# Optimization experiments

Measured on AMD Instinct MI355X. Metric: run time of the kernel, lower is better.

## Reference

```python
import jax, jax.numpy as jnp
import numpy as np
import math

INPUT_SIZE = 512
DK = 64
B, N = 8, 2048

def setup_inputs() -> dict:
    key = jax.random.key(0)
    k1, k2, k3, k4, k5, k6 = jax.random.split(key, 6)
    X = jax.random.normal(k1, (B, N, INPUT_SIZE), dtype=jnp.float32)
    h = jax.random.normal(k2, (B, N, INPUT_SIZE), dtype=jnp.float32)
    s = 1.0 / math.sqrt(INPUT_SIZE)
    WQ = jax.random.uniform(k3, (INPUT_SIZE, DK), dtype=jnp.float32, minval=-s, maxval=s)
    bQ = jax.random.uniform(k4, (DK,), dtype=jnp.float32, minval=-s, maxval=s)
    WK = jax.random.uniform(k5, (INPUT_SIZE, DK), dtype=jnp.float32, minval=-s, maxval=s)
    bK = jax.random.uniform(k6, (DK,), dtype=jnp.float32, minval=-s, maxval=s)
    return {"X": X, "h": h, "WQ": WQ, "bQ": bQ, "WK": WK, "bK": bK}

def reference(X, h, WQ, bQ, WK, bK):
    # Q = linearQ(h), K = linearK(X); dropout is eval-mode identity
    Q = jnp.einsum('bnd,dk->bnk', h, WQ) + bQ   # [B, N, dk]
    K = jnp.einsum('bnd,dk->bnk', X, WK) + bK   # [B, N, dk]
    scores = jnp.einsum('bqk,bnk->bqn', Q, K) / jnp.sqrt(jnp.asarray(DK, X.dtype))
    A = jax.nn.softmax(scores, axis=-1)          # [B, N, N]
    out = jnp.einsum('bqn,bnd->bqd', A, X)       # V = X
    return out
```

## Files before the change

kernel.cpp:

```cpp
#include <hip/hip_runtime.h>
#include <hip/hip_bf16.h>

#define B_ 8
#define N_ 2048
#define D_ 512
#define DK_ 64

typedef float f32x4 __attribute__((ext_vector_type(4)));
typedef short bf16x8 __attribute__((ext_vector_type(8)));
typedef unsigned short u16;

__device__ __forceinline__ u16 f2bf(float f) {
  union { float f; unsigned u; } v; v.f = f;
  unsigned r = v.u + 0x7FFFu + ((v.u >> 16) & 1u);
  return (u16)(r >> 16);
}

#define MFMA16(a, b, cacc) __builtin_amdgcn_mfma_f32_16x16x32_bf16((a), (b), (cacc), 0, 0, 0)


__global__ __launch_bounds__(256) void vt_kernel(const float* __restrict__ X,
                                                 u16* __restrict__ Vf) {
  int bid = blockIdx.x;
  int dt = bid & 7, nt = (bid >> 3) & 31, b = bid >> 8;
  int n0 = nt * 64, d0 = dt * 64;
  __shared__ u16 T[64 * 72];
  int t = threadIdx.x;
  const float* Xb = X + ((size_t)b * N_ + n0) * D_ + d0;
#pragma unroll
  for (int p = 0; p < 4; ++p) {
    int r = p * 16 + (t >> 4);
    int c4 = (t & 15) * 4;
    f32x4 v = *reinterpret_cast<const f32x4*>(Xb + (size_t)r * D_ + c4);
#pragma unroll
    for (int j = 0; j < 4; ++j) T[(c4 + j) * 72 + r] = f2bf(v[j]);
  }
  __syncthreads();
  int w = t >> 6, l = t & 63, g = l >> 4, c = l & 15;
#pragma unroll
  for (int ks = 0; ks < 2; ++ks) {
    bf16x8 v = *reinterpret_cast<const bf16x8*>(&T[(w * 16 + c) * 72 + ks * 32 + 8 * g]);
    *reinterpret_cast<bf16x8*>(
        Vf + (((size_t)(b * 32 + dt * 4 + w) * 32 + nt) * 2 + ks) * 512 + l * 8) = v;
  }
}

__global__ __launch_bounds__(256) void proj_kernel(
    const float* __restrict__ h, const float* __restrict__ X,
    const float* __restrict__ WQ, const float* __restrict__ bQ,
    const float* __restrict__ WK, const float* __restrict__ bK,
    u16* __restrict__ Qf, u16* __restrict__ Kf) {
  int bid = blockIdx.x;
  int b = bid & 7, nt = bid >> 3;
  int n0 = nt * 64;
  int t = threadIdx.x, w = t >> 6, l = t & 63, g = l >> 4, c = l & 15;
  int arow = n0 + w * 16 + c;
  const float* hrow = h + ((size_t)b * N_ + arow) * D_;
  const float* Xrow = X + ((size_t)b * N_ + arow) * D_;
  f32x4 accq[4], acck[4];
#pragma unroll
  for (int cf = 0; cf < 4; ++cf) {
    accq[cf] = (f32x4){0.f, 0.f, 0.f, 0.f};
    acck[cf] = (f32x4){0.f, 0.f, 0.f, 0.f};
  }
  for (int k0 = 0; k0 < D_; k0 += 32) {
    bf16x8 ah, ax;
    {
      f32x4 h0 = *reinterpret_cast<const f32x4*>(hrow + k0 + 8 * g);
      f32x4 h1 = *reinterpret_cast<const f32x4*>(hrow + k0 + 8 * g + 4);
      f32x4 x0 = *reinterpret_cast<const f32x4*>(Xrow + k0 + 8 * g);
      f32x4 x1 = *reinterpret_cast<const f32x4*>(Xrow + k0 + 8 * g + 4);
#pragma unroll
      for (int i = 0; i < 4; ++i) {
        ah[i] = (short)f2bf(h0[i]); ah[i + 4] = (short)f2bf(h1[i]);
        ax[i] = (short)f2bf(x0[i]); ax[i + 4] = (short)f2bf(x1[i]);
      }
    }
#pragma unroll
    for (int cf = 0; cf < 4; ++cf) {
      bf16x8 bq, bk;
#pragma unroll
      for (int i = 0; i < 8; ++i) {
        int kk = k0 + 8 * g + i;
        bq[i] = (short)f2bf(WQ[(size_t)kk * DK_ + cf * 16 + c]);
        bk[i] = (short)f2bf(WK[(size_t)kk * DK_ + cf * 16 + c]);
      }
      accq[cf] = MFMA16(ah, bq, accq[cf]);
      acck[cf] = MFMA16(ax, bk, acck[cf]);
    }
  }
#pragma unroll
  for (int cf = 0; cf < 4; ++cf) {
    float vq = bQ[cf * 16 + c], vk = bK[cf * 16 + c];
    int ks = cf >> 1;
    int g2 = ((cf & 1) * 16 + c) >> 3;
    int i2 = c & 7;
#pragma unroll
    for (int r = 0; r < 4; ++r) {
      size_t e = ((size_t)(b * 128 + nt * 4 + w) * 2 + ks) * 512 +
                 (g2 * 16 + 4 * g + r) * 8 + i2;
      Qf[e] = f2bf((accq[cf][r] + vq) * 0.125f);
      Kf[e] = f2bf(acck[cf][r] + vk);
    }
  }
}

__global__ __launch_bounds__(512, 1) void attn_kernel(
    const u16* __restrict__ Qf, const u16* __restrict__ Kf,
    const u16* __restrict__ Vf, float* __restrict__ out) {
  int bid = blockIdx.x;
  int b = bid & 7, qt = bid >> 3;
  int q0 = qt * 64;
  int t = threadIdx.x, w = t >> 6, l = t & 63, g = l >> 4, c = l & 15;
  int qh = w >> 2, kq = w & 3;

  __shared__ u16 Plds[2][64][72];
  __shared__ float Lp[4][64];

  bf16x8 aq[2][2];
#pragma unroll
  for (int qf = 0; qf < 2; ++qf)
#pragma unroll
    for (int ks = 0; ks < 2; ++ks)
      aq[qf][ks] = *reinterpret_cast<const bf16x8*>(
          Qf + ((size_t)(b * 128 + qt * 4 + qh * 2 + qf) * 2 + ks) * 512 + l * 8);

  f32x4 o[4][4];
#pragma unroll
  for (int a = 0; a < 4; ++a)
#pragma unroll
    for (int d = 0; d < 4; ++d) o[a][d] = (f32x4){0.f, 0.f, 0.f, 0.f};
  float lp[2][4];
#pragma unroll
  for (int a = 0; a < 2; ++a)
#pragma unroll
    for (int r = 0; r < 4; ++r) lp[a][r] = 0.f;

  const u16* Kbase = Kf + (size_t)(b * 128 + kq) * 2 * 512 + l * 8;
  const u16* Vbase = Vf + ((size_t)(b * 32 + w * 4) * 32) * 2 * 512 + l * 8;

  bf16x8 vA[8], vB[8], kA[2], kB[2];
#pragma unroll
  for (int ks = 0; ks < 2; ++ks) {
    kA[ks] = *reinterpret_cast<const bf16x8*>(Kbase + (size_t)ks * 512);
#pragma unroll
    for (int df = 0; df < 4; ++df)
      vA[ks * 4 + df] = *reinterpret_cast<const bf16x8*>(
          Vbase + ((size_t)df * 32 * 2 + ks) * 512);
  }

  auto body = [&](bf16x8 (&vC)[8], bf16x8 (&kC)[2],
                  bf16x8 (&vN)[8], bf16x8 (&kN)[2], int i) {
    const int pb = i & 1;
    const int kvn = (i + 1) & 31;

#pragma unroll
    for (int ks = 0; ks < 2; ++ks) {
      kN[ks] = *reinterpret_cast<const bf16x8*>(
          Kbase + ((size_t)kvn * 4 * 2 + ks) * 512);
#pragma unroll
      for (int df = 0; df < 4; ++df)
        vN[ks * 4 + df] = *reinterpret_cast<const bf16x8*>(
            Vbase + (((size_t)df * 32 + kvn) * 2 + ks) * 512);
    }

    f32x4 s0 = (f32x4){0.f, 0.f, 0.f, 0.f};
    f32x4 s1 = (f32x4){0.f, 0.f, 0.f, 0.f};
    s0 = MFMA16(aq[0][0], kC[0], s0); s0 = MFMA16(aq[0][1], kC[1], s0);
    s1 = MFMA16(aq[1][0], kC[0], s1); s1 = MFMA16(aq[1][1], kC[1], s1);

#pragma unroll
    for (int r = 0; r < 4; ++r) {
      float p0 = __expf(s0[r]); lp[0][r] += p0;
      Plds[pb][qh * 32 + 4 * g + r][kq * 16 + c] = f2bf(p0);
      float p1 = __expf(s1[r]); lp[1][r] += p1;
      Plds[pb][qh * 32 + 16 + 4 * g + r][kq * 16 + c] = f2bf(p1);
    }

    __syncthreads();

#pragma unroll
    for (int ks = 0; ks < 2; ++ks) {
      bf16x8 pa0 = *reinterpret_cast<const bf16x8*>(&Plds[pb][c][ks * 32 + 8 * g]);
      bf16x8 pa1 = *reinterpret_cast<const bf16x8*>(&Plds[pb][16 + c][ks * 32 + 8 * g]);
      bf16x8 pa2 = *reinterpret_cast<const bf16x8*>(&Plds[pb][32 + c][ks * 32 + 8 * g]);
      bf16x8 pa3 = *reinterpret_cast<const bf16x8*>(&Plds[pb][48 + c][ks * 32 + 8 * g]);
#pragma unroll
      for (int df = 0; df < 4; ++df) {
        o[0][df] = MFMA16(pa0, vC[ks * 4 + df], o[0][df]);
        o[1][df] = MFMA16(pa1, vC[ks * 4 + df], o[1][df]);
        o[2][df] = MFMA16(pa2, vC[ks * 4 + df], o[2][df]);
        o[3][df] = MFMA16(pa3, vC[ks * 4 + df], o[3][df]);
      }
    }
  };

#pragma unroll 1
  for (int i = 0; i < 32; i += 2) {
    body(vA, kA, vB, kB, i);
    body(vB, kB, vA, kA, i + 1);
  }

#pragma unroll
  for (int qf = 0; qf < 2; ++qf)
#pragma unroll
    for (int r = 0; r < 4; ++r) {
      float v = lp[qf][r];
      v += __shfl_xor(v, 1); v += __shfl_xor(v, 2);
      v += __shfl_xor(v, 4); v += __shfl_xor(v, 8);
      lp[qf][r] = v;
    }
  if (c == 0) {
#pragma unroll
    for (int qf = 0; qf < 2; ++qf)
#pragma unroll
      for (int r = 0; r < 4; ++r)
        Lp[kq][qh * 32 + qf * 16 + 4 * g + r] = lp[qf][r];
  }
  __syncthreads();

  float* outb = out + ((size_t)b * N_ + q0) * D_;
#pragma unroll
  for (int qf2 = 0; qf2 < 4; ++qf2)
#pragma unroll
    for (int r = 0; r < 4; ++r) {
      int ql = qf2 * 16 + 4 * g + r;
      float L = Lp[0][ql] + Lp[1][ql] + Lp[2][ql] + Lp[3][ql];
      float inv = 1.0f / L;
#pragma unroll
      for (int df = 0; df < 4; ++df)
        outb[(size_t)ql * D_ + w * 64 + df * 16 + c] = o[qf2][df][r] * inv;
    }
}

extern "C" void kernel_launch(void* const* d_in, const int* in_sizes, int n_in,
                              void* d_out, int out_size, void* d_ws, size_t ws_size,
                              hipStream_t stream) {
  const float* X  = (const float*)d_in[0];
  const float* h  = (const float*)d_in[1];
  const float* WQ = (const float*)d_in[2];
  const float* bQ = (const float*)d_in[3];
  const float* WK = (const float*)d_in[4];
  const float* bK = (const float*)d_in[5];
  float* out = (float*)d_out;

  u16* Vf = (u16*)d_ws;
  u16* Qf = Vf + (size_t)B_ * D_ * N_;
  u16* Kf = Qf + (size_t)B_ * N_ * DK_;

  vt_kernel<<<dim3(2048), dim3(256), 0, stream>>>(X, Vf);
  proj_kernel<<<dim3(256), dim3(256), 0, stream>>>(h, X, WQ, bQ, WK, bK, Qf, Kf);
  attn_kernel<<<dim3(256), dim3(512), 0, stream>>>(Qf, Kf, Vf, out);
}
```

Measured before the change: 81.34 us.

## Compute transposed scores in registers to drop LDS round-trip and barriers for P

```diff
diff --git a/kernel.cpp b/kernel.cpp
--- a/kernel.cpp
+++ b/kernel.cpp
@@ -8,6 +8,9 @@
 
 typedef float f32x4 __attribute__((ext_vector_type(4)));
 typedef short bf16x8 __attribute__((ext_vector_type(8)));
+typedef short bf16x4 __attribute__((ext_vector_type(4)));
+typedef unsigned int uint2v __attribute__((ext_vector_type(2)));
+typedef unsigned long long u64x2 __attribute__((ext_vector_type(2)));
 typedef unsigned short u16;
 
 __device__ __forceinline__ u16 f2bf(float f) {
@@ -16,14 +19,21 @@
   return (u16)(r >> 16);
 }
 
-#define MFMA16(a, b, cacc) __builtin_amdgcn_mfma_f32_16x16x32_bf16((a), (b), (cacc), 0, 0, 0)
+#define MFMA32(a, b, cacc) __builtin_amdgcn_mfma_f32_16x16x32_bf16((a), (b), (cacc), 0, 0, 0)
+#define MFMA16(a, b, cacc) __builtin_amdgcn_mfma_f32_16x16x16bf16_1k((a), (b), (cacc), 0, 0, 0)
+
+__device__ __forceinline__ unsigned cvt_pk_bf16(float lo, float hi) {
+  unsigned r;
+  asm("v_cvt_pk_bf16_f32 %0, %1, %2" : "=v"(r) : "v"(lo), "v"(hi));
+  return r;
+}
 
 
 __global__ __launch_bounds__(256) void vt_kernel(const float* __restrict__ X,
                                                  u16* __restrict__ Vf) {
   int bid = blockIdx.x;
-  int dt = bid & 7, nt = (bid >> 3) & 31, b = bid >> 8;
-  int n0 = nt * 64, d0 = dt * 64;
+  int dt8 = bid & 7, nt = (bid >> 3) & 31, b = bid >> 8;
+  int n0 = nt * 64, d0 = dt8 * 64;
   __shared__ u16 T[64 * 72];
   int t = threadIdx.x;
   const float* Xb = X + ((size_t)b * N_ + n0) * D_ + d0;
@@ -38,10 +48,15 @@
   __syncthreads();
   int w = t >> 6, l = t & 63, g = l >> 4, c = l & 15;
 #pragma unroll
-  for (int ks = 0; ks < 2; ++ks) {
-    bf16x8 v = *reinterpret_cast<const bf16x8*>(&T[(w * 16 + c) * 72 + ks * 32 + 8 * g]);
+  for (int jl = 0; jl < 2; ++jl) {
+    u64x2 tmp;
+    tmp[0] = *reinterpret_cast<const unsigned long long*>(
+        &T[(w * 16 + c) * 72 + jl * 32 + 4 * g]);
+    tmp[1] = *reinterpret_cast<const unsigned long long*>(
+        &T[(w * 16 + c) * 72 + jl * 32 + 16 + 4 * g]);
+    bf16x8 v = __builtin_bit_cast(bf16x8, tmp);
     *reinterpret_cast<bf16x8*>(
-        Vf + (((size_t)(b * 32 + dt * 4 + w) * 32 + nt) * 2 + ks) * 512 + l * 8) = v;
+        Vf + (((size_t)(b * 32 + dt8 * 4 + w) * 64) + nt * 2 + jl) * 512 + l * 8) = v;
   }
 }
 
@@ -85,8 +100,8 @@
         bq[i] = (short)f2bf(WQ[(size_t)kk * DK_ + cf * 16 + c]);
         bk[i] = (short)f2bf(WK[(size_t)kk * DK_ + cf * 16 + c]);
       }
-      accq[cf] = MFMA16(ah, bq, accq[cf]);
-      acck[cf] = MFMA16(ax, bk, acck[cf]);
+      accq[cf] = MFMA32(ah, bq, accq[cf]);
+      acck[cf] = MFMA32(ax, bk, acck[cf]);
     }
   }
 #pragma unroll
@@ -105,131 +120,120 @@
   }
 }
 
-__global__ __launch_bounds__(512, 1) void attn_kernel(
+__global__ __launch_bounds__(512, 2) void attn_kernel(
     const u16* __restrict__ Qf, const u16* __restrict__ Kf,
     const u16* __restrict__ Vf, float* __restrict__ out) {
   int bid = blockIdx.x;
   int b = bid & 7, qt = bid >> 3;
   int q0 = qt * 64;
   int t = threadIdx.x, w = t >> 6, l = t & 63, g = l >> 4, c = l & 15;
-  int qh = w >> 2, kq = w & 3;
-
-  __shared__ u16 Plds[2][64][72];
-  __shared__ float Lp[4][64];
-
-  bf16x8 aq[2][2];
-#pragma unroll
-  for (int qf = 0; qf < 2; ++qf)
+
+  __shared__ float Lsh[8][64];
+
+  bf16x8 aq[4][2];
+#pragma unroll
+  for (int sl = 0; sl < 4; ++sl)
 #pragma unroll
     for (int ks = 0; ks < 2; ++ks)
-      aq[qf][ks] = *reinterpret_cast<const bf16x8*>(
-          Qf + ((size_t)(b * 128 + qt * 4 + qh * 2 + qf) * 2 + ks) * 512 + l * 8);
+      aq[sl][ks] = *reinterpret_cast<const bf16x8*>(
+          Qf + ((size_t)(b * 128 + qt * 4 + sl) * 2 + ks) * 512 + l * 8);
 
   f32x4 o[4][4];
 #pragma unroll
-  for (int a = 0; a < 4; ++a)
-#pragma unroll
-    for (int d = 0; d < 4; ++d) o[a][d] = (f32x4){0.f, 0.f, 0.f, 0.f};
-  float lp[2][4];
-#pragma unroll
-  for (int a = 0; a < 2; ++a)
-#pragma unroll
-    for (int r = 0; r < 4; ++r) lp[a][r] = 0.f;
-
-  const u16* Kbase = Kf + (size_t)(b * 128 + kq) * 2 * 512 + l * 8;
-  const u16* Vbase = Vf + ((size_t)(b * 32 + w * 4) * 32) * 2 * 512 + l * 8;
-
-  bf16x8 vA[8], vB[8], kA[2], kB[2];
-#pragma unroll
-  for (int ks = 0; ks < 2; ++ks) {
-    kA[ks] = *reinterpret_cast<const bf16x8*>(Kbase + (size_t)ks * 512);
-#pragma unroll
-    for (int df = 0; df < 4; ++df)
-      vA[ks * 4 + df] = *reinterpret_cast<const bf16x8*>(
-          Vbase + ((size_t)df * 32 * 2 + ks) * 512);
-  }
-
-  auto body = [&](bf16x8 (&vC)[8], bf16x8 (&kC)[2],
-                  bf16x8 (&vN)[8], bf16x8 (&kN)[2], int i) {
-    const int pb = i & 1;
-    const int kvn = (i + 1) & 31;
-
-#pragma unroll
-    for (int ks = 0; ks < 2; ++ks) {
-      kN[ks] = *reinterpret_cast<const bf16x8*>(
-          Kbase + ((size_t)kvn * 4 * 2 + ks) * 512);
+  for (int sl = 0; sl < 4; ++sl)
+#pragma unroll
+    for (int df = 0; df < 4; ++df) o[sl][df] = (f32x4){0.f, 0.f, 0.f, 0.f};
+  float lp[4] = {0.f, 0.f, 0.f, 0.f};
+
+  const u16* Kbase = Kf + ((size_t)b * 256) * 512 + l * 8;
+  const u16* Vbase = Vf + ((size_t)(b * 32 + w * 4) * 64) * 512 + l * 8;
+
+  bf16x8 kA[4], kB[4], vA[4], vB[4];
+
+#define LOADW(kT, vT, j)                                                      \
+  do {                                                                        \
+    _Pragma("unroll") for (int kv2 = 0; kv2 < 4; ++kv2)                       \
+        kT[kv2] = *reinterpret_cast<const bf16x8*>(                           \
+            Kbase + (size_t)(((j) * 2 + (kv2 >> 1)) * 2 + (kv2 & 1)) * 512);  \
+    _Pragma("unroll") for (int df = 0; df < 4; ++df)                          \
+        vT[df] = *reinterpret_cast<const bf16x8*>(                            \
+            Vbase + (size_t)(df * 64 + (j)) * 512);                           \
+  } while (0)
+
+  LOADW(kA, vA, 0);
+
+  auto body = [&](bf16x8 (&kC)[4], bf16x8 (&vC)[4],
+                  bf16x8 (&kN)[4], bf16x8 (&vN)[4], int i) {
+    const int jn = (i + 1) & 63;
+    LOADW(kN, vN, jn);
+
+    f32x4 s[2][4];
+#pragma unroll
+    for (int kvh = 0; kvh < 2; ++kvh)
+#pragma unroll
+      for (int sl = 0; sl < 4; ++sl) {
+        s[kvh][sl] = (f32x4){0.f, 0.f, 0.f, 0.f};
+        s[kvh][sl] = MFMA32(kC[kvh * 2 + 0], aq[sl][0], s[kvh][sl]);
+        s[kvh][sl] = MFMA32(kC[kvh * 2 + 1], aq[sl][1], s[kvh][sl]);
+      }
+
+    bf16x4 pa[2][4];
+#pragma unroll
+    for (int kvh = 0; kvh < 2; ++kvh)
+#pragma unroll
+      for (int sl = 0; sl < 4; ++sl) {
+        float p0 = __expf(s[kvh][sl][0]), p1 = __expf(s[kvh][sl][1]);
+        float p2 = __expf(s[kvh][sl][2]), p3 = __expf(s[kvh][sl][3]);
+        lp[sl] += (p0 + p1) + (p2 + p3);
+        unsigned r0 = cvt_pk_bf16(p0, p1), r1 = cvt_pk_bf16(p2, p3);
+        uint2v u = {r0, r1};
+        pa[kvh][sl] = __builtin_bit_cast(bf16x4, u);
+      }
+
+    __builtin_amdgcn_s_setprio(1);
+#pragma unroll
+    for (int df = 0; df < 4; ++df) {
+      bf16x4 vlo = __builtin_shufflevector(vC[df], vC[df], 0, 1, 2, 3);
+      bf16x4 vhi = __builtin_shufflevector(vC[df], vC[df], 4, 5, 6, 7);
+#pragma unroll
+      for (int sl = 0; sl < 4; ++sl) {
+        o[sl][df] = MFMA16(pa[0][sl], vlo, o[sl][df]);
+        o[sl][df] = MFMA16(pa[1][sl], vhi, o[sl][df]);
+      }
+    }
+    __builtin_amdgcn_s_setprio(0);
+  };
+
+#pragma unroll 1
+  for (int i = 0; i < 64; i += 2) {
+    body(kA, vA, kB, vB, i);
+    body(kB, vB, kA, vA, i + 1);
+  }
+#undef LOADW
+
+#pragma unroll
+  for (int sl = 0; sl < 4; ++sl) {
+    float v = lp[sl];
+    v += __shfl_xor(v, 16);
+    v += __shfl_xor(v, 32);
+    lp[sl] = v;
+  }
+  if (l < 16) {
+#pragma unroll
+    for (int sl = 0; sl < 4; ++sl) Lsh[w][sl * 16 + l] = lp[sl];
+  }
+  __syncthreads();
+
+  float* outb = out + ((size_t)b * N_ + q0) * D_;
+#pragma unroll
+  for (int sl = 0; sl < 4; ++sl)
+#pragma unroll
+    for (int r = 0; r < 4; ++r) {
+      float inv = 1.0f / Lsh[w][sl * 16 + 4 * g + r];
+      int q = sl * 16 + 4 * g + r;
 #pragma unroll
       for (int df = 0; df < 4; ++df)
-        vN[ks * 4 + df] = *reinterpret_cast<const bf16x8*>(
-            Vbase + (((size_t)df * 32 + kvn) * 2 + ks) * 512);
-    }
-
-    f32x4 s0 = (f32x4){0.f, 0.f, 0.f, 0.f};
-    f32x4 s1 = (f32x4){0.f, 0.f, 0.f, 0.f};
-    s0 = MFMA16(aq[0][0], kC[0], s0); s0 = MFMA16(aq[0][1], kC[1], s0);
-    s1 = MFMA16(aq[1][0], kC[0], s1); s1 = MFMA16(aq[1][1], kC[1], s1);
-
-#pragma unroll
-    for (int r = 0; r < 4; ++r) {
-      float p0 = __expf(s0[r]); lp[0][r] += p0;
-      Plds[pb][qh * 32 + 4 * g + r][kq * 16 + c] = f2bf(p0);
-      float p1 = __expf(s1[r]); lp[1][r] += p1;
-      Plds[pb][qh * 32 + 16 + 4 * g + r][kq * 16 + c] = f2bf(p1);
-    }
-
-    __syncthreads();
-
-#pragma unroll
-    for (int ks = 0; ks < 2; ++ks) {
-      bf16x8 pa0 = *reinterpret_cast<const bf16x8*>(&Plds[pb][c][ks * 32 + 8 * g]);
-      bf16x8 pa1 = *reinterpret_cast<const bf16x8*>(&Plds[pb][16 + c][ks * 32 + 8 * g]);
-      bf16x8 pa2 = *reinterpret_cast<const bf16x8*>(&Plds[pb][32 + c][ks * 32 + 8 * g]);
-      bf16x8 pa3 = *reinterpret_cast<const bf16x8*>(&Plds[pb][48 + c][ks * 32 + 8 * g]);
-#pragma unroll
-      for (int df = 0; df < 4; ++df) {
-        o[0][df] = MFMA16(pa0, vC[ks * 4 + df], o[0][df]);
-        o[1][df] = MFMA16(pa1, vC[ks * 4 + df], o[1][df]);
-        o[2][df] = MFMA16(pa2, vC[ks * 4 + df], o[2][df]);
-        o[3][df] = MFMA16(pa3, vC[ks * 4 + df], o[3][df]);
-      }
-    }
-  };
-
-#pragma unroll 1
-  for (int i = 0; i < 32; i += 2) {
-    body(vA, kA, vB, kB, i);
-    body(vB, kB, vA, kA, i + 1);
-  }
-
-#pragma unroll
-  for (int qf = 0; qf < 2; ++qf)
-#pragma unroll
-    for (int r = 0; r < 4; ++r) {
-      float v = lp[qf][r];
-      v += __shfl_xor(v, 1); v += __shfl_xor(v, 2);
-      v += __shfl_xor(v, 4); v += __shfl_xor(v, 8);
-      lp[qf][r] = v;
-    }
-  if (c == 0) {
-#pragma unroll
-    for (int qf = 0; qf < 2; ++qf)
-#pragma unroll
-      for (int r = 0; r < 4; ++r)
-        Lp[kq][qh * 32 + qf * 16 + 4 * g + r] = lp[qf][r];
-  }
-  __syncthreads();
-
-  float* outb = out + ((size_t)b * N_ + q0) * D_;
-#pragma unroll
-  for (int qf2 = 0; qf2 < 4; ++qf2)
-#pragma unroll
-    for (int r = 0; r < 4; ++r) {
-      int ql = qf2 * 16 + 4 * g + r;
-      float L = Lp[0][ql] + Lp[1][ql] + Lp[2][ql] + Lp[3][ql];
-      float inv = 1.0f / L;
-#pragma unroll
-      for (int df = 0; df < 4; ++df)
-        outb[(size_t)ql * D_ + w * 64 + df * 16 + c] = o[qf2][df][r] * inv;
+        outb[(size_t)q * D_ + w * 64 + df * 16 + c] = o[sl][df][r] * inv;
     }
 }
 
```

Result: slower. 117.3 us (+44.2%).
